# Optimization experiments

Measured on AMD Instinct MI355X. Metric: run time of the kernel, lower is better.

The kernel has to match this reference:

```python
import jax, jax.numpy as jnp
import numpy as np

B, NQ, NK = 2, 1024, 8192
DIM, CTX_DIM = 512, 512
HEADS, DIM_HEAD = 8, 64
INNER = HEADS * DIM_HEAD
EPS = 1e-5
SCALE = DIM_HEAD ** -0.5


def layernorm(x, w, b):
    m = jnp.mean(x, axis=-1, keepdims=True)
    v = jnp.var(x, axis=-1, keepdims=True)
    return (x - m) * jax.lax.rsqrt(v + EPS) * w + b


def rotate_half(x):
    # interleaved pairs: (..., 2i, 2i+1) -> (-x[2i+1], x[2i])
    x1 = x[..., 0::2]
    x2 = x[..., 1::2]
    return jnp.stack((-x2, x1), axis=-1).reshape(x.shape)


def apply_rope(freqs, x):
    # freqs: (b, n, d) broadcast over heads; x: (b, h, n, d)
    f = freqs[:, None, :, :]
    return x * jnp.cos(f) + rotate_half(x) * jnp.sin(f)


def setup_inputs() -> dict:
    key = jax.random.key(0)
    ks = jax.random.split(key, 12)
    x_query = jax.random.normal(ks[0], (B, NQ, DIM), jnp.float32)
    x_context = jax.random.normal(ks[1], (B, NK, CTX_DIM), jnp.float32)
    rotary_q = jax.random.uniform(ks[2], (B, NQ, DIM_HEAD), jnp.float32) * 6.28
    rotary_c = jax.random.uniform(ks[3], (B, NK, DIM_HEAD), jnp.float32) * 6.28
    attn_mask = jax.random.uniform(ks[4], (B, NK)) > 0.1
    attn_mask = attn_mask.at[:, 0].set(True)  # ensure >=1 valid key per row
    s_q = (1.0 / DIM) ** 0.5
    s_c = (1.0 / CTX_DIM) ** 0.5
    s_o = (1.0 / INNER) ** 0.5
    return {
        'x_query': x_query,
        'x_context': x_context,
        'rotary_q': rotary_q,
        'rotary_c': rotary_c,
        'attn_mask': attn_mask,
        'norm_w': jnp.ones((DIM,), jnp.float32),
        'norm_b': jnp.zeros((DIM,), jnp.float32),
        'norm_ctx_w': jnp.ones((CTX_DIM,), jnp.float32),
        'norm_ctx_b': jnp.zeros((CTX_DIM,), jnp.float32),
        'w_q': jax.random.uniform(ks[5], (DIM, INNER), jnp.float32, -s_q, s_q),
        'w_kv': jax.random.uniform(ks[6], (CTX_DIM, 2 * INNER), jnp.float32, -s_c, s_c),
        'w_out': jax.random.uniform(ks[7], (INNER, DIM), jnp.float32, -s_o, s_o),
        'b_out': jax.random.uniform(ks[8], (DIM,), jnp.float32, -s_o, s_o),
    }


def reference(x_query, x_context, rotary_q, rotary_c, attn_mask,
              norm_w, norm_b, norm_ctx_w, norm_ctx_b, w_q, w_kv, w_out, b_out):
    xq = layernorm(x_query, norm_w, norm_b)
    xc = layernorm(x_context, norm_ctx_w, norm_ctx_b)
    q = jnp.einsum('bnd,de->bne', xq, w_q)
    kv = jnp.einsum('bnd,de->bne', xc, w_kv)
    k, v = jnp.split(kv, 2, axis=-1)
    split_heads = lambda t: t.reshape(t.shape[0], t.shape[1], HEADS, DIM_HEAD).transpose(0, 2, 1, 3)
    q, k, v = split_heads(q), split_heads(k), split_heads(v)
    q = apply_rope(rotary_q, q)
    k = apply_rope(rotary_c, k)
    v = apply_rope(rotary_c, v)  # rotate_value=True
    scores = jnp.einsum('bhqd,bhkd->bhqk', q, k) * SCALE
    scores = jnp.where(attn_mask[:, None, None, :], scores, jnp.finfo(scores.dtype).min)
    attn = jax.nn.softmax(scores, axis=-1)
    out = jnp.einsum('bhqk,bhkd->bhqd', attn, v)
    out = apply_rope(-rotary_q, out)  # inverse rotation of output
    out = out.transpose(0, 2, 1, 3).reshape(out.shape[0], NQ, INNER)
    return jnp.einsum('bne,ed->bnd', out, w_out) + b_out
```

## Files before the change

kernel.cpp:

```cpp
#include <hip/hip_runtime.h>
#include <math.h>

typedef __attribute__((ext_vector_type(8))) short  short8;
typedef __attribute__((ext_vector_type(4))) float  f32x4;
typedef __attribute__((ext_vector_type(4))) unsigned short u16x4;
typedef __attribute__((ext_vector_type(8))) unsigned short u16x8;
typedef unsigned short u16;

#define B_     2
#define NQ_    1024
#define NK_    8192
#define DIM_   512
#define H_     8
#define DH_    64
#define EPS_   1e-5f
#define SCALE_ 0.125f
#define LOG2E_ 1.4426950408889634f
#define SPLITS 4

__device__ __forceinline__ u16 f2bf(float f) {
  unsigned int u = __float_as_uint(f);
  u += 0x7fffu + ((u >> 16) & 1u);
  return (u16)(u >> 16);
}
__device__ __forceinline__ float fmax3(float a, float b, float c) {
  return fmaxf(fmaxf(a, b), c);
}

__global__ __launch_bounds__(256) void wt_kernel(
    const float* __restrict__ wq, const float* __restrict__ wkv,
    const float* __restrict__ wout,
    u16* __restrict__ wqT, u16* __restrict__ wkvT, u16* __restrict__ woutT) {
  __shared__ float tile[64][65];
  int bid = blockIdx.x;
  const float* W; u16* WT; int N; int tix;
  if (bid < 64)       { W = wq;   WT = wqT;   N = 512;  tix = bid; }
  else if (bid < 192) { W = wkv;  WT = wkvT;  N = 1024; tix = bid - 64; }
  else                { W = wout; WT = woutT; N = 512;  tix = bid - 192; }
  int ntn = N >> 6;
  int k0 = (tix / ntn) << 6, n0 = (tix % ntn) << 6;
  int t = threadIdx.x;
  {
    int kk = t >> 2, nc = (t & 3) << 4;
#pragma unroll
    for (int i = 0; i < 4; ++i) {
      f32x4 v = *(const f32x4*)&W[(size_t)(k0 + kk) * N + n0 + nc + 4 * i];
      tile[kk][nc + 4*i + 0] = v[0];
      tile[kk][nc + 4*i + 1] = v[1];
      tile[kk][nc + 4*i + 2] = v[2];
      tile[kk][nc + 4*i + 3] = v[3];
    }
  }
  __syncthreads();
  {
    int n = t >> 2, kc = (t & 3) << 4;
#pragma unroll
    for (int i = 0; i < 2; ++i) {
      u16x8 o;
#pragma unroll
      for (int j = 0; j < 8; ++j) o[j] = f2bf(tile[kc + 8*i + j][n]);
      *(u16x8*)&WT[(size_t)(n0 + n) * 512 + k0 + kc + 8*i] = o;
    }
  }
}

__global__ __launch_bounds__(256) void ln_kernel(
    const float* __restrict__ xq, const float* __restrict__ xc,
    const float* __restrict__ nw, const float* __restrict__ nb,
    const float* __restrict__ ncw, const float* __restrict__ ncb,
    u16* __restrict__ xqb, u16* __restrict__ xcb) {
  int wid = threadIdx.x >> 6, lane = threadIdx.x & 63;
  int row = blockIdx.x * 4 + wid;
  const float* x; const float* w; const float* bb; u16* o; int r;
  if (row < 2048) { x = xq; w = nw;  bb = nb;  o = xqb; r = row; }
  else            { x = xc; w = ncw; bb = ncb; o = xcb; r = row - 2048; }
  const f32x4* px = (const f32x4*)(x + (size_t)r * 512);
  f32x4 v0 = px[lane], v1 = px[lane + 64];
  float s  = v0[0]+v0[1]+v0[2]+v0[3] + v1[0]+v1[1]+v1[2]+v1[3];
  float ss = v0[0]*v0[0]+v0[1]*v0[1]+v0[2]*v0[2]+v0[3]*v0[3]
           + v1[0]*v1[0]+v1[1]*v1[1]+v1[2]*v1[2]+v1[3]*v1[3];
#pragma unroll
  for (int ofs = 32; ofs >= 1; ofs >>= 1) { s += __shfl_xor(s, ofs); ss += __shfl_xor(ss, ofs); }
  float mu = s * (1.f/512.f);
  float var = ss * (1.f/512.f) - mu*mu;
  float rs = rsqrtf(var + EPS_);
  const f32x4* pw = (const f32x4*)w; const f32x4* pb = (const f32x4*)bb;
#pragma unroll
  for (int seg = 0; seg < 2; ++seg) {
    int e4 = lane + 64*seg;
    f32x4 xv = seg ? v1 : v0;
    f32x4 wv = pw[e4], bv = pb[e4];
    u16x4 ov;
#pragma unroll
    for (int c = 0; c < 4; ++c) ov[c] = f2bf((xv[c]-mu)*rs*wv[c] + bv[c]);
    *(u16x4*)&o[(size_t)r*512 + e4*4] = ov;
  }
}

__global__ __launch_bounds__(256) void trig_kernel(
    const float* __restrict__ rq, const float* __restrict__ rc,
    float* __restrict__ cq, float* __restrict__ sq,
    float* __restrict__ cc, float* __restrict__ sc) {
  int i = blockIdx.x * 256 + threadIdx.x;
  const int NQE = B_*NQ_*DH_;
  const int NCE = B_*NK_*DH_;
  if (i < NQE) { float s, c; sincosf(rq[i], &s, &c); cq[i] = c; sq[i] = s; }
  if (i < NCE) { float s, c; sincosf(rc[i], &s, &c); cc[i] = c; sc[i] = s; }
}

template<int MODE>
__global__ __launch_bounds__(256) void gemm_mfma(
    const u16* __restrict__ Abf, const u16* __restrict__ WT,
    const float* __restrict__ ctab, const float* __restrict__ stab,
    const float* __restrict__ bias,
    u16* __restrict__ out0, u16* __restrict__ out1, float* __restrict__ outf) {
  constexpr int BM   = (MODE==1) ? 128 : 64;
  constexpr int BN   = (MODE==1) ? 128 : 32;
  constexpr int MR   = BM/64;
  constexpr int NR   = BN/16;
  constexpr int N    = (MODE==1) ? 1024 : 512;
  constexpr int NSEQ = (MODE==1) ? 8192 : 1024;
  constexpr int NBN  = N / BN;
  constexpr int NWG  = (((MODE==1)?16384:2048)/BM) * NBN;
  __shared__ u16 As[BM*64];
  __shared__ u16 Bs[BN*64];
  const int tid = threadIdx.x;
  const int w = tid >> 6, l = tid & 63;
  const int la = l >> 4, lb = l & 15;
  int bid = blockIdx.x;
  bid = (bid & 7) * (NWG/8) + (bid >> 3);
  const int m0 = (bid / NBN) * BM;
  const int n0 = (bid % NBN) * BN;
  f32x4 acc[MR][NR];
#pragma unroll
  for (int i = 0; i < MR; ++i)
#pragma unroll
    for (int j = 0; j < NR; ++j) acc[i][j] = (f32x4){0.f,0.f,0.f,0.f};

  constexpr int APT = BM/32;
  constexpr int BPT = BN/32;
  const int arow = tid / (8/APT);
  const int ag0  = (tid % (8/APT)) * APT;
  const int brow = tid / (8/BPT);
  const int bg0  = (tid % (8/BPT)) * BPT;

  auto loadA = [&](int k0, int g) -> short8 {
    if (MODE == 2) {
      int kk = k0 + g*8;
      int m = m0 + arow;
      return *(const short8*)&Abf[((size_t)((m >> 10)*H_ + (kk >> 6)) * NQ_ + (m & 1023)) * 64 + (kk & 63)];
    } else {
      return *(const short8*)&Abf[(size_t)(m0 + arow) * 512 + k0 + g*8];
    }
  };

  short8 apre[APT], bpre[BPT];
#pragma unroll
  for (int i = 0; i < APT; ++i) apre[i] = loadA(0, ag0 + i);
#pragma unroll
  for (int i = 0; i < BPT; ++i) bpre[i] = *(const short8*)&WT[(size_t)(n0 + brow) * 512 + (bg0 + i)*8];

  for (int k0 = 0; k0 < 512; k0 += 64) {
    if (k0) __syncthreads();
#pragma unroll
    for (int i = 0; i < APT; ++i) {
      int g = ag0 + i;
      *(short8*)&As[arow*64 + ((g ^ (arow & 7)) << 3)] = apre[i];
    }
#pragma unroll
    for (int i = 0; i < BPT; ++i) {
      int g = bg0 + i;
      *(short8*)&Bs[brow*64 + ((g ^ (brow & 7)) << 3)] = bpre[i];
    }
    if (k0 + 64 < 512) {
#pragma unroll
      for (int i = 0; i < APT; ++i) apre[i] = loadA(k0 + 64, ag0 + i);
#pragma unroll
      for (int i = 0; i < BPT; ++i) bpre[i] = *(const short8*)&WT[(size_t)(n0 + brow) * 512 + (k0+64) + (bg0 + i)*8];
    }
    __syncthreads();
#pragma unroll
    for (int h = 0; h < 2; ++h) {
      short8 af[MR], bfr[NR];
#pragma unroll
      for (int i = 0; i < MR; ++i) {
        int row = w*(16*MR) + i*16 + lb;
        int g = (4*h + la) ^ (row & 7);
        af[i] = *(const short8*)&As[row*64 + g*8];
      }
#pragma unroll
      for (int j = 0; j < NR; ++j) {
        int row = j*16 + lb;
        int g = (4*h + la) ^ (row & 7);
        bfr[j] = *(const short8*)&Bs[row*64 + g*8];
      }
#pragma unroll
      for (int i = 0; i < MR; ++i)
#pragma unroll
        for (int j = 0; j < NR; ++j)
          acc[i][j] = __builtin_amdgcn_mfma_f32_16x16x32_bf16(af[i], bfr[j], acc[i][j], 0, 0, 0);
    }
  }

  if (MODE == 2) {
#pragma unroll
    for (int i = 0; i < MR; ++i)
#pragma unroll
      for (int j = 0; j < NR; ++j) {
        int n = n0 + 16*j + lb;
        float bv = bias[n];
#pragma unroll
        for (int r = 0; r < 4; ++r) {
          int m = m0 + w*(16*MR) + 16*i + 4*la + r;
          outf[(size_t)m * 512 + n] = acc[i][j][r] + bv;
        }
      }
  } else if (MODE == 1 && n0 >= 512) {
#pragma unroll
    for (int i = 0; i < MR; ++i)
#pragma unroll
      for (int j = 0; j < NR; ++j) {
        int n = n0 + 16*j + lb;
        int e = n - 512, hh = e >> 6, dh = e & 63;
        int mbase = m0 + w*(16*MR) + 16*i + 4*la;
        int bI = mbase / NSEQ;
        int seq = mbase - bI*NSEQ;
        u16x4 pk4;
#pragma unroll
        for (int r = 0; r < 4; ++r) {
          int m = mbase + r;
          float x = acc[i][j][r];
          float pr = __shfl_xor(x, 1);
          float cv = ctab[(size_t)m*64 + dh];
          float sv = stab[(size_t)m*64 + dh];
          pk4[r] = f2bf(x*cv + ((n & 1) ? pr*sv : -pr*sv));
        }
        *(u16x4*)&out1[((size_t)(bI*H_ + hh)*64 + dh)*8192 + seq] = pk4;
      }
  } else {
#pragma unroll
    for (int i = 0; i < MR; ++i)
#pragma unroll
      for (int j = 0; j < NR; ++j) {
        int n = n0 + 16*j + lb;
        int hh = n >> 6, dh = n & 63;
#pragma unroll
        for (int r = 0; r < 4; ++r) {
          int m = m0 + w*(16*MR) + 16*i + 4*la + r;
          float x = acc[i][j][r];
          float pr = __shfl_xor(x, 1);
          float cv = ctab[(size_t)m*64 + dh];
          float sv = stab[(size_t)m*64 + dh];
          float y = x*cv + ((n & 1) ? pr*sv : -pr*sv);
          if (MODE == 0) y *= SCALE_ * LOG2E_;
          int bI = m / NSEQ, seq = m % NSEQ;
          out0[((size_t)(bI*H_ + hh) * NSEQ + seq) * 64 + dh] = f2bf(y);
        }
      }
  }
}

__global__ __launch_bounds__(512) void attn_mfma(
    const u16* __restrict__ qb, const u16* __restrict__ kb,
    const u16* __restrict__ vtg, const int* __restrict__ mask,
    float* __restrict__ Opart, float* __restrict__ mpart, float* __restrict__ lpart) {
  __shared__ u16 Ks[64*64];
  __shared__ u16 Vt[64*64];
  __shared__ u16 Ps[8*16*64];
  __shared__ float Mskf[2048];
  int bid = blockIdx.x;
  bid = (bid & 7) * 64 + (bid >> 3);
  const int s  = bid & (SPLITS-1);
  const int qt = (bid >> 2) & 7;
  const int bh = bid >> 5;
  const int bI = bh >> 3;
  const int tid = threadIdx.x;
  const int w = tid >> 6, l = tid & 63;
  const int la = l >> 4, lb = l & 15;
  const int key0 = s * (NK_/SPLITS);

#pragma unroll
  for (int i = 0; i < 4; ++i)
    Mskf[i*512 + tid] = mask[bI*NK_ + key0 + i*512 + tid] ? 0.f : -1e30f;

  const int qrow = qt*128 + w*16 + lb;
  short8 qf0 = *(const short8*)&qb[(((size_t)bh * NQ_) + qrow) * 64 + 8*la];
  short8 qf1 = *(const short8*)&qb[(((size_t)bh * NQ_) + qrow) * 64 + 32 + 8*la];

  const int krow = tid >> 3;
  const int kg   = tid & 7;
  const u16* kptr = kb  + ((size_t)bh * NK_ + key0 + krow) * 64;
  const u16* vptr = vtg + ((size_t)bh * 64 + krow) * 8192 + key0;
  short8 kpre = *(const short8*)&kptr[kg*8];
  short8 vpre = *(const short8*)&vptr[kg*8];
  const int ksw = krow & 7;

  f32x4 accO[4];
#pragma unroll
  for (int j = 0; j < 4; ++j) accO[j] = (f32x4){0.f,0.f,0.f,0.f};
  float m_run = -1e30f, l_run = 0.f;
  constexpr int NT = (NK_/SPLITS)/64;

  const int pbase = (w*16 + lb)*64;
  const int pwofs = (4*la) & 7;

  for (int kt = 0; kt < NT; ++kt) {
    *(short8*)&Ks[krow*64 + ((kg ^ ksw) << 3)] = kpre;
    *(short8*)&Vt[krow*64 + ((kg ^ ksw) << 3)] = vpre;
    if (kt + 1 < NT) {
      kpre = *(const short8*)&kptr[(kt+1)*4096 + kg*8];
      vpre = *(const short8*)&vptr[(kt+1)*64 + kg*8];
    }
    __syncthreads();

    f32x4 sc[4];
#pragma unroll
    for (int t = 0; t < 4; ++t) sc[t] = (f32x4){0.f,0.f,0.f,0.f};
    __builtin_amdgcn_s_setprio(1);
#pragma unroll
    for (int t = 0; t < 4; ++t) {
      int row = t*16 + lb;
      int g0 = la ^ (row & 7);
      int g1 = (4 + la) ^ (row & 7);
      short8 kf0 = *(const short8*)&Ks[row*64 + g0*8];
      short8 kf1 = *(const short8*)&Ks[row*64 + g1*8];
      sc[t] = __builtin_amdgcn_mfma_f32_16x16x32_bf16(kf0, qf0, sc[t], 0, 0, 0);
      sc[t] = __builtin_amdgcn_mfma_f32_16x16x32_bf16(kf1, qf1, sc[t], 0, 0, 0);
    }
    __builtin_amdgcn_s_setprio(0);
    float sv[16];
#pragma unroll
    for (int t = 0; t < 4; ++t) {
      f32x4 mk = *(const f32x4*)&Mskf[kt*64 + t*16 + 4*la];
#pragma unroll
      for (int r = 0; r < 4; ++r) sv[4*t+r] = sc[t][r] + mk[r];
    }
    float a0 = fmax3(sv[0],  sv[1],  sv[2]);
    float a1 = fmax3(sv[3],  sv[4],  sv[5]);
    float a2 = fmax3(sv[6],  sv[7],  sv[8]);
    float a3 = fmax3(sv[9],  sv[10], sv[11]);
    float a4 = fmax3(sv[12], sv[13], sv[14]);
    float pmax = fmaxf(fmax3(a0, a1, a2), fmax3(a3, a4, sv[15]));
    pmax = fmaxf(pmax, __shfl_xor(pmax, 16));
    pmax = fmaxf(pmax, __shfl_xor(pmax, 32));
    if (!__all(pmax <= m_run + 11.f)) {
      float mnew = fmaxf(m_run, pmax);
      float scl = __builtin_amdgcn_exp2f(m_run - mnew);
      m_run = mnew;
      l_run *= scl;
      float sr[4];
#pragma unroll
      for (int r = 0; r < 4; ++r) sr[r] = __shfl(scl, (l & 48) | (4*la + r));
#pragma unroll
      for (int j = 0; j < 4; ++j)
#pragma unroll
        for (int r = 0; r < 4; ++r) accO[j][r] *= sr[r];
    }
    float p[16];
    float psum = 0.f;
#pragma unroll
    for (int i = 0; i < 16; ++i) {
      p[i] = __builtin_amdgcn_exp2f(sv[i] - m_run);
      psum += p[i];
    }
    psum += __shfl_xor(psum, 16);
    psum += __shfl_xor(psum, 32);
    l_run += psum;
#pragma unroll
    for (int t = 0; t < 4; ++t) {
      int gst = 2*t + (la >> 1);
      uint2 pp;
      asm("v_cvt_pk_bf16_f32 %0, %1, %2" : "=v"(pp.x) : "v"(p[4*t+0]), "v"(p[4*t+1]));
      asm("v_cvt_pk_bf16_f32 %0, %1, %2" : "=v"(pp.y) : "v"(p[4*t+2]), "v"(p[4*t+3]));
      *(uint2*)&Ps[pbase + ((gst ^ (lb & 7)) << 3) + pwofs] = pp;
    }
    __builtin_amdgcn_s_setprio(1);
#pragma unroll
    for (int kh = 0; kh < 2; ++kh) {
      int pg = (4*kh + la) ^ (lb & 7);
      short8 pf = *(const short8*)&Ps[pbase + pg*8];
#pragma unroll
      for (int j = 0; j < 4; ++j) {
        int d = j*16 + lb;
        int vg = (4*kh + la) ^ (d & 7);
        short8 vf = *(const short8*)&Vt[d*64 + vg*8];
        accO[j] = __builtin_amdgcn_mfma_f32_16x16x32_bf16(pf, vf, accO[j], 0, 0, 0);
      }
    }
    __builtin_amdgcn_s_setprio(0);
    __syncthreads();
  }

  const int qa = qt*128 + w*16;
  const size_t obase = ((size_t)s*16 + bh) * 1024;
#pragma unroll
  for (int j = 0; j < 4; ++j)
#pragma unroll
    for (int r = 0; r < 4; ++r)
      Opart[(obase + qa + 4*la + r) * 64 + j*16 + lb] = accO[j][r];
  if (la == 0) {
    mpart[obase + qa + lb] = m_run;
    lpart[obase + qa + lb] = l_run;
  }
}

__global__ __launch_bounds__(256) void combine_kernel(
    const float* __restrict__ Opart, const float* __restrict__ mpart,
    const float* __restrict__ lpart,
    const float* __restrict__ cosq, const float* __restrict__ sinq,
    u16* __restrict__ aob) {
  const int bid = blockIdx.x;
  const int bh = bid >> 4, qt = bid & 15;
  const int t = threadIdx.x;
  const int ql = t >> 2, ds = (t & 3) << 4;
  const int q = qt*64 + ql;
  const int bI = bh >> 3;
  const size_t rbase = ((size_t)bh << 10) + q;
  float m[SPLITS], li[SPLITS];
  float M = -1e30f;
#pragma unroll
  for (int s = 0; s < SPLITS; ++s) {
    m[s]  = mpart[(size_t)s*16384 + rbase];
    li[s] = lpart[(size_t)s*16384 + rbase];
    M = fmaxf(M, m[s]);
  }
  float ws[SPLITS]; float den = 0.f;
#pragma unroll
  for (int s = 0; s < SPLITS; ++s) { ws[s] = __builtin_amdgcn_exp2f(m[s] - M); den += ws[s]*li[s]; }
  float inv = 1.f / den;
  u16 ob[16];
#pragma unroll
  for (int c = 0; c < 4; ++c) {
    int d0 = ds + 4*c;
    f32x4 o = (f32x4){0.f,0.f,0.f,0.f};
#pragma unroll
    for (int s = 0; s < SPLITS; ++s) {
      f32x4 v = *(const f32x4*)&Opart[((size_t)s*16384 + rbase)*64 + d0];
      o += ws[s] * v;
    }
    o *= inv;
    size_t tix = ((((size_t)bI << 10) + q) << 6) + d0;
    f32x4 cv = *(const f32x4*)&cosq[tix];
    f32x4 sv = *(const f32x4*)&sinq[tix];
    ob[4*c+0] = f2bf(o[0]*cv[0] + o[1]*sv[0]);
    ob[4*c+1] = f2bf(o[1]*cv[1] - o[0]*sv[1]);
    ob[4*c+2] = f2bf(o[2]*cv[2] + o[3]*sv[2]);
    ob[4*c+3] = f2bf(o[3]*cv[3] - o[2]*sv[3]);
  }
  u16x8 w0, w1;
#pragma unroll
  for (int j = 0; j < 8; ++j) { w0[j] = ob[j]; w1[j] = ob[8+j]; }
  *(u16x8*)&aob[rbase*64 + ds]     = w0;
  *(u16x8*)&aob[rbase*64 + ds + 8] = w1;
}

extern "C" void kernel_launch(void* const* d_in, const int* in_sizes, int n_in,
                              void* d_out, int out_size, void* d_ws, size_t ws_size,
                              hipStream_t stream) {
  (void)in_sizes; (void)n_in; (void)out_size; (void)ws_size;
  const float* xq   = (const float*)d_in[0];
  const float* xc   = (const float*)d_in[1];
  const float* rq   = (const float*)d_in[2];
  const float* rc   = (const float*)d_in[3];
  const int*   mask = (const int*)d_in[4];
  const float* nw   = (const float*)d_in[5];
  const float* nb   = (const float*)d_in[6];
  const float* ncw  = (const float*)d_in[7];
  const float* ncb  = (const float*)d_in[8];
  const float* wq   = (const float*)d_in[9];
  const float* wkv  = (const float*)d_in[10];
  const float* wout = (const float*)d_in[11];
  const float* bout = (const float*)d_in[12];
  float* out = (float*)d_out;

  char* p = (char*)d_ws;
  u16* wqT   = (u16*)p;  p += 524288;
  u16* wkvT  = (u16*)p;  p += 1048576;
  u16* woutT = (u16*)p;  p += 524288;
  u16* xqb   = (u16*)p;  p += 2097152;
  u16* xcb   = (u16*)p;  p += 16777216;
  float* cosq = (float*)p; p += 524288;
  float* sinq = (float*)p; p += 524288;
  float* cosc = (float*)p; p += 4194304;
  float* sinc = (float*)p; p += 4194304;
  u16* qb  = (u16*)p; p += 2097152;
  u16* kb  = (u16*)p; p += 16777216;
  u16* vtg = (u16*)p; p += 16777216;
  float* mpart = (float*)p; p += 262144;
  float* lpart = (float*)p; p += 262144;
  u16* aob = (u16*)p; p += 2097152;
  float* Opart = (float*)xcb;

  wt_kernel<<<dim3(256), dim3(256), 0, stream>>>(wq, wkv, wout, wqT, wkvT, woutT);
  ln_kernel<<<dim3(4608), dim3(256), 0, stream>>>(xq, xc, nw, nb, ncw, ncb, xqb, xcb);
  trig_kernel<<<dim3(4096), dim3(256), 0, stream>>>(rq, rc, cosq, sinq, cosc, sinc);
  gemm_mfma<0><<<dim3(512), dim3(256), 0, stream>>>(
      xqb, wqT, cosq, sinq, nullptr, qb, nullptr, nullptr);
  gemm_mfma<1><<<dim3(1024), dim3(256), 0, stream>>>(
      xcb, wkvT, cosc, sinc, nullptr, kb, vtg, nullptr);
  attn_mfma<<<dim3(16*8*SPLITS), dim3(512), 0, stream>>>(
      qb, kb, vtg, mask, Opart, mpart, lpart);
  combine_kernel<<<dim3(256), dim3(256), 0, stream>>>(
      Opart, mpart, lpart, cosq, sinq, aob);
  gemm_mfma<2><<<dim3(512), dim3(256), 0, stream>>>(
      aob, woutT, nullptr, nullptr, bout, nullptr, nullptr, out);
}
```

Measured before the change: 213.0 us.

## Fuse prep kernels, fold key mask into V, and use 8-way KV split

```diff
diff --git a/kernel.cpp b/kernel.cpp
--- a/kernel.cpp
+++ b/kernel.cpp
@@ -16,7 +16,6 @@
 #define EPS_   1e-5f
 #define SCALE_ 0.125f
 #define LOG2E_ 1.4426950408889634f
-#define SPLITS 4
 
 __device__ __forceinline__ u16 f2bf(float f) {
   unsigned int u = __float_as_uint(f);
@@ -27,92 +26,95 @@
   return fmaxf(fmaxf(a, b), c);
 }
 
-__global__ __launch_bounds__(256) void wt_kernel(
+__global__ __launch_bounds__(256) void prep_kernel(
     const float* __restrict__ wq, const float* __restrict__ wkv,
     const float* __restrict__ wout,
-    u16* __restrict__ wqT, u16* __restrict__ wkvT, u16* __restrict__ woutT) {
-  __shared__ float tile[64][65];
-  int bid = blockIdx.x;
-  const float* W; u16* WT; int N; int tix;
-  if (bid < 64)       { W = wq;   WT = wqT;   N = 512;  tix = bid; }
-  else if (bid < 192) { W = wkv;  WT = wkvT;  N = 1024; tix = bid - 64; }
-  else                { W = wout; WT = woutT; N = 512;  tix = bid - 192; }
-  int ntn = N >> 6;
-  int k0 = (tix / ntn) << 6, n0 = (tix % ntn) << 6;
-  int t = threadIdx.x;
-  {
-    int kk = t >> 2, nc = (t & 3) << 4;
-#pragma unroll
-    for (int i = 0; i < 4; ++i) {
-      f32x4 v = *(const f32x4*)&W[(size_t)(k0 + kk) * N + n0 + nc + 4 * i];
-      tile[kk][nc + 4*i + 0] = v[0];
-      tile[kk][nc + 4*i + 1] = v[1];
-      tile[kk][nc + 4*i + 2] = v[2];
-      tile[kk][nc + 4*i + 3] = v[3];
-    }
-  }
-  __syncthreads();
-  {
-    int n = t >> 2, kc = (t & 3) << 4;
-#pragma unroll
-    for (int i = 0; i < 2; ++i) {
-      u16x8 o;
-#pragma unroll
-      for (int j = 0; j < 8; ++j) o[j] = f2bf(tile[kc + 8*i + j][n]);
-      *(u16x8*)&WT[(size_t)(n0 + n) * 512 + k0 + kc + 8*i] = o;
-    }
-  }
-}
-
-__global__ __launch_bounds__(256) void ln_kernel(
     const float* __restrict__ xq, const float* __restrict__ xc,
     const float* __restrict__ nw, const float* __restrict__ nb,
     const float* __restrict__ ncw, const float* __restrict__ ncb,
-    u16* __restrict__ xqb, u16* __restrict__ xcb) {
-  int wid = threadIdx.x >> 6, lane = threadIdx.x & 63;
-  int row = blockIdx.x * 4 + wid;
-  const float* x; const float* w; const float* bb; u16* o; int r;
-  if (row < 2048) { x = xq; w = nw;  bb = nb;  o = xqb; r = row; }
-  else            { x = xc; w = ncw; bb = ncb; o = xcb; r = row - 2048; }
-  const f32x4* px = (const f32x4*)(x + (size_t)r * 512);
-  f32x4 v0 = px[lane], v1 = px[lane + 64];
-  float s  = v0[0]+v0[1]+v0[2]+v0[3] + v1[0]+v1[1]+v1[2]+v1[3];
-  float ss = v0[0]*v0[0]+v0[1]*v0[1]+v0[2]*v0[2]+v0[3]*v0[3]
-           + v1[0]*v1[0]+v1[1]*v1[1]+v1[2]*v1[2]+v1[3]*v1[3];
-#pragma unroll
-  for (int ofs = 32; ofs >= 1; ofs >>= 1) { s += __shfl_xor(s, ofs); ss += __shfl_xor(ss, ofs); }
-  float mu = s * (1.f/512.f);
-  float var = ss * (1.f/512.f) - mu*mu;
-  float rs = rsqrtf(var + EPS_);
-  const f32x4* pw = (const f32x4*)w; const f32x4* pb = (const f32x4*)bb;
-#pragma unroll
-  for (int seg = 0; seg < 2; ++seg) {
-    int e4 = lane + 64*seg;
-    f32x4 xv = seg ? v1 : v0;
-    f32x4 wv = pw[e4], bv = pb[e4];
-    u16x4 ov;
-#pragma unroll
-    for (int c = 0; c < 4; ++c) ov[c] = f2bf((xv[c]-mu)*rs*wv[c] + bv[c]);
-    *(u16x4*)&o[(size_t)r*512 + e4*4] = ov;
-  }
-}
-
-__global__ __launch_bounds__(256) void trig_kernel(
     const float* __restrict__ rq, const float* __restrict__ rc,
-    float* __restrict__ cq, float* __restrict__ sq,
-    float* __restrict__ cc, float* __restrict__ sc) {
-  int i = blockIdx.x * 256 + threadIdx.x;
-  const int NQE = B_*NQ_*DH_;
-  const int NCE = B_*NK_*DH_;
-  if (i < NQE) { float s, c; sincosf(rq[i], &s, &c); cq[i] = c; sq[i] = s; }
-  if (i < NCE) { float s, c; sincosf(rc[i], &s, &c); cc[i] = c; sc[i] = s; }
+    const int* __restrict__ mask,
+    u16* __restrict__ wqT, u16* __restrict__ wkvT, u16* __restrict__ woutT,
+    u16* __restrict__ xqb, u16* __restrict__ xcb,
+    float* __restrict__ cq, float* __restrict__ sq2,
+    float* __restrict__ cc, float* __restrict__ sc2,
+    float* __restrict__ maskf) {
+  __shared__ float tile[64][65];
+  const int bid = blockIdx.x;
+  const int t = threadIdx.x;
+  if (bid < 256) {
+    const float* W; u16* WT; int N; int tix;
+    if (bid < 64)       { W = wq;   WT = wqT;   N = 512;  tix = bid; }
+    else if (bid < 192) { W = wkv;  WT = wkvT;  N = 1024; tix = bid - 64; }
+    else                { W = wout; WT = woutT; N = 512;  tix = bid - 192; }
+    int ntn = N >> 6;
+    int k0 = (tix / ntn) << 6, n0 = (tix % ntn) << 6;
+    {
+      int kk = t >> 2, nc = (t & 3) << 4;
+#pragma unroll
+      for (int i = 0; i < 4; ++i) {
+        f32x4 v = *(const f32x4*)&W[(size_t)(k0 + kk) * N + n0 + nc + 4 * i];
+        tile[kk][nc + 4*i + 0] = v[0];
+        tile[kk][nc + 4*i + 1] = v[1];
+        tile[kk][nc + 4*i + 2] = v[2];
+        tile[kk][nc + 4*i + 3] = v[3];
+      }
+    }
+    __syncthreads();
+    {
+      int n = t >> 2, kc = (t & 3) << 4;
+#pragma unroll
+      for (int i = 0; i < 2; ++i) {
+        u16x8 o;
+#pragma unroll
+        for (int j = 0; j < 8; ++j) o[j] = f2bf(tile[kc + 8*i + j][n]);
+        *(u16x8*)&WT[(size_t)(n0 + n) * 512 + k0 + kc + 8*i] = o;
+      }
+    }
+  } else if (bid < 4864) {
+    int wid = t >> 6, lane = t & 63;
+    int row = (bid - 256) * 4 + wid;
+    const float* x; const float* w; const float* bb; u16* o; int r;
+    if (row < 2048) { x = xq; w = nw;  bb = nb;  o = xqb; r = row; }
+    else            { x = xc; w = ncw; bb = ncb; o = xcb; r = row - 2048; }
+    const f32x4* px = (const f32x4*)(x + (size_t)r * 512);
+    f32x4 v0 = px[lane], v1 = px[lane + 64];
+    float s  = v0[0]+v0[1]+v0[2]+v0[3] + v1[0]+v1[1]+v1[2]+v1[3];
+    float ss = v0[0]*v0[0]+v0[1]*v0[1]+v0[2]*v0[2]+v0[3]*v0[3]
+             + v1[0]*v1[0]+v1[1]*v1[1]+v1[2]*v1[2]+v1[3]*v1[3];
+#pragma unroll
+    for (int ofs = 32; ofs >= 1; ofs >>= 1) { s += __shfl_xor(s, ofs); ss += __shfl_xor(ss, ofs); }
+    float mu = s * (1.f/512.f);
+    float var = ss * (1.f/512.f) - mu*mu;
+    float rs = rsqrtf(var + EPS_);
+    const f32x4* pw = (const f32x4*)w; const f32x4* pb = (const f32x4*)bb;
+#pragma unroll
+    for (int seg = 0; seg < 2; ++seg) {
+      int e4 = lane + 64*seg;
+      f32x4 xv = seg ? v1 : v0;
+      f32x4 wv = pw[e4], bv = pb[e4];
+      u16x4 ov;
+#pragma unroll
+      for (int c = 0; c < 4; ++c) ov[c] = f2bf((xv[c]-mu)*rs*wv[c] + bv[c]);
+      *(u16x4*)&o[(size_t)r*512 + e4*4] = ov;
+    }
+  } else if (bid < 8960) {
+    int i = (bid - 4864) * 256 + t;
+    const int NQE = B_*NQ_*DH_;
+    const int NCE = B_*NK_*DH_;
+    if (i < NQE) { float s, c; sincosf(rq[i], &s, &c); cq[i] = c; sq2[i] = s; }
+    if (i < NCE) { float s, c; sincosf(rc[i], &s, &c); cc[i] = c; sc2[i] = s; }
+  } else {
+    int i = (bid - 8960) * 256 + t;
+    maskf[i] = mask[i] ? 1.f : 0.f;
+  }
 }
 
 template<int MODE>
 __global__ __launch_bounds__(256) void gemm_mfma(
     const u16* __restrict__ Abf, const u16* __restrict__ WT,
     const float* __restrict__ ctab, const float* __restrict__ stab,
-    const float* __restrict__ bias,
+    const float* __restrict__ bias, const float* __restrict__ mvf,
     u16* __restrict__ out0, u16* __restrict__ out1, float* __restrict__ outf) {
   constexpr int BM   = (MODE==1) ? 128 : 64;
   constexpr int BN   = (MODE==1) ? 128 : 32;
@@ -217,14 +219,15 @@
       }
   } else if (MODE == 1 && n0 >= 512) {
 #pragma unroll
-    for (int i = 0; i < MR; ++i)
+    for (int i = 0; i < MR; ++i) {
+      int mbase = m0 + w*(16*MR) + 16*i + 4*la;
+      int bI = mbase >> 13;
+      int seq = mbase & 8191;
+      f32x4 mkv = *(const f32x4*)&mvf[mbase];
 #pragma unroll
       for (int j = 0; j < NR; ++j) {
         int n = n0 + 16*j + lb;
         int e = n - 512, hh = e >> 6, dh = e & 63;
-        int mbase = m0 + w*(16*MR) + 16*i + 4*la;
-        int bI = mbase / NSEQ;
-        int seq = mbase - bI*NSEQ;
         u16x4 pk4;
 #pragma unroll
         for (int r = 0; r < 4; ++r) {
@@ -233,10 +236,11 @@
           float pr = __shfl_xor(x, 1);
           float cv = ctab[(size_t)m*64 + dh];
           float sv = stab[(size_t)m*64 + dh];
-          pk4[r] = f2bf(x*cv + ((n & 1) ? pr*sv : -pr*sv));
+          pk4[r] = f2bf((x*cv + ((n & 1) ? pr*sv : -pr*sv)) * mkv[r]);
         }
         *(u16x4*)&out1[((size_t)(bI*H_ + hh)*64 + dh)*8192 + seq] = pk4;
       }
+    }
   } else {
 #pragma unroll
     for (int i = 0; i < MR; ++i)
@@ -260,28 +264,27 @@
   }
 }
 
+template<int NS>
 __global__ __launch_bounds__(512) void attn_mfma(
     const u16* __restrict__ qb, const u16* __restrict__ kb,
-    const u16* __restrict__ vtg, const int* __restrict__ mask,
+    const u16* __restrict__ vtg, const float* __restrict__ maskf,
     float* __restrict__ Opart, float* __restrict__ mpart, float* __restrict__ lpart) {
   __shared__ u16 Ks[64*64];
   __shared__ u16 Vt[64*64];
   __shared__ u16 Ps[8*16*64];
-  __shared__ float Mskf[2048];
-  int bid = blockIdx.x;
-  bid = (bid & 7) * 64 + (bid >> 3);
-  const int s  = bid & (SPLITS-1);
-  const int qt = (bid >> 2) & 7;
-  const int bh = bid >> 5;
+  constexpr int NWG = 16*8*NS;
+  constexpr int CH  = NWG/8;
+  constexpr int LS  = (NS==8) ? 3 : 2;
+  int orig = blockIdx.x;
+  int wid = (orig & 7) * CH + (orig >> 3);
+  const int qt = wid & 7;
+  const int s  = (wid >> 3) & (NS-1);
+  const int bh = wid >> (3 + LS);
   const int bI = bh >> 3;
   const int tid = threadIdx.x;
   const int w = tid >> 6, l = tid & 63;
   const int la = l >> 4, lb = l & 15;
-  const int key0 = s * (NK_/SPLITS);
-
-#pragma unroll
-  for (int i = 0; i < 4; ++i)
-    Mskf[i*512 + tid] = mask[bI*NK_ + key0 + i*512 + tid] ? 0.f : -1e30f;
+  const int key0 = s * (NK_/NS);
 
   const int qrow = qt*128 + w*16 + lb;
   short8 qf0 = *(const short8*)&qb[(((size_t)bh * NQ_) + qrow) * 64 + 8*la];
@@ -294,12 +297,13 @@
   short8 kpre = *(const short8*)&kptr[kg*8];
   short8 vpre = *(const short8*)&vptr[kg*8];
   const int ksw = krow & 7;
+  const float* mrow = maskf + bI*8192 + key0 + 4*la;
 
   f32x4 accO[4];
 #pragma unroll
   for (int j = 0; j < 4; ++j) accO[j] = (f32x4){0.f,0.f,0.f,0.f};
   float m_run = -1e30f, l_run = 0.f;
-  constexpr int NT = (NK_/SPLITS)/64;
+  constexpr int NT = (NK_/NS)/64;
 
   const int pbase = (w*16 + lb)*64;
   const int pwofs = (4*la) & 7;
@@ -328,19 +332,12 @@
       sc[t] = __builtin_amdgcn_mfma_f32_16x16x32_bf16(kf1, qf1, sc[t], 0, 0, 0);
     }
     __builtin_amdgcn_s_setprio(0);
-    float sv[16];
-#pragma unroll
-    for (int t = 0; t < 4; ++t) {
-      f32x4 mk = *(const f32x4*)&Mskf[kt*64 + t*16 + 4*la];
-#pragma unroll
-      for (int r = 0; r < 4; ++r) sv[4*t+r] = sc[t][r] + mk[r];
-    }
-    float a0 = fmax3(sv[0],  sv[1],  sv[2]);
-    float a1 = fmax3(sv[3],  sv[4],  sv[5]);
-    float a2 = fmax3(sv[6],  sv[7],  sv[8]);
-    float a3 = fmax3(sv[9],  sv[10], sv[11]);
-    float a4 = fmax3(sv[12], sv[13], sv[14]);
-    float pmax = fmaxf(fmax3(a0, a1, a2), fmax3(a3, a4, sv[15]));
+    float a0 = fmax3(sc[0][0], sc[0][1], sc[0][2]);
+    float a1 = fmax3(sc[0][3], sc[1][0], sc[1][1]);
+    float a2 = fmax3(sc[1][2], sc[1][3], sc[2][0]);
+    float a3 = fmax3(sc[2][1], sc[2][2], sc[2][3]);
+    float a4 = fmax3(sc[3][0], sc[3][1], sc[3][2]);
+    float pmax = fmaxf(fmax3(a0, a1, a2), fmax3(a3, a4, sc[3][3]));
     pmax = fmaxf(pmax, __shfl_xor(pmax, 16));
     pmax = fmaxf(pmax, __shfl_xor(pmax, 32));
     if (!__all(pmax <= m_run + 11.f)) {
@@ -356,24 +353,25 @@
 #pragma unroll
         for (int r = 0; r < 4; ++r) accO[j][r] *= sr[r];
     }
-    float p[16];
-    float psum = 0.f;
-#pragma unroll
-    for (int i = 0; i < 16; ++i) {
-      p[i] = __builtin_amdgcn_exp2f(sv[i] - m_run);
-      psum += p[i];
-    }
-    psum += __shfl_xor(psum, 16);
-    psum += __shfl_xor(psum, 32);
-    l_run += psum;
+    float l_add = 0.f;
 #pragma unroll
     for (int t = 0; t < 4; ++t) {
+      f32x4 mk = *(const f32x4*)&mrow[kt*64 + t*16];
+      float p0 = __builtin_amdgcn_exp2f(sc[t][0] - m_run);
+      float p1 = __builtin_amdgcn_exp2f(sc[t][1] - m_run);
+      float p2 = __builtin_amdgcn_exp2f(sc[t][2] - m_run);
+      float p3 = __builtin_amdgcn_exp2f(sc[t][3] - m_run);
+      l_add = fmaf(p0, mk[0], l_add);
+      l_add = fmaf(p1, mk[1], l_add);
+      l_add = fmaf(p2, mk[2], l_add);
+      l_add = fmaf(p3, mk[3], l_add);
       int gst = 2*t + (la >> 1);
       uint2 pp;
-      asm("v_cvt_pk_bf16_f32 %0, %1, %2" : "=v"(pp.x) : "v"(p[4*t+0]), "v"(p[4*t+1]));
-      asm("v_cvt_pk_bf16_f32 %0, %1, %2" : "=v"(pp.y) : "v"(p[4*t+2]), "v"(p[4*t+3]));
+      asm("v_cvt_pk_bf16_f32 %0, %1, %2" : "=v"(pp.x) : "v"(p0), "v"(p1));
+      asm("v_cvt_pk_bf16_f32 %0, %1, %2" : "=v"(pp.y) : "v"(p2), "v"(p3));
       *(uint2*)&Ps[pbase + ((gst ^ (lb & 7)) << 3) + pwofs] = pp;
     }
+    l_run += l_add;
     __builtin_amdgcn_s_setprio(1);
 #pragma unroll
     for (int kh = 0; kh < 2; ++kh) {
@@ -391,6 +389,9 @@
     __syncthreads();
   }
 
+  l_run += __shfl_xor(l_run, 16);
+  l_run += __shfl_xor(l_run, 32);
+
   const int qa = qt*128 + w*16;
   const size_t obase = ((size_t)s*16 + bh) * 1024;
 #pragma unroll
@@ -404,6 +405,7 @@
   }
 }
 
+template<int NS>
 __global__ __launch_bounds__(256) void combine_kernel(
     const float* __restrict__ Opart, const float* __restrict__ mpart,
     const float* __restrict__ lpart,
@@ -416,17 +418,17 @@
   const int q = qt*64 + ql;
   const int bI = bh >> 3;
   const size_t rbase = ((size_t)bh << 10) + q;
-  float m[SPLITS], li[SPLITS];
+  float m[NS], li[NS];
   float M = -1e30f;
 #pragma unroll
-  for (int s = 0; s < SPLITS; ++s) {
+  for (int s = 0; s < NS; ++s) {
     m[s]  = mpart[(size_t)s*16384 + rbase];
     li[s] = lpart[(size_t)s*16384 + rbase];
     M = fmaxf(M, m[s]);
   }
-  float ws[SPLITS]; float den = 0.f;
-#pragma unroll
-  for (int s = 0; s < SPLITS; ++s) { ws[s] = __builtin_amdgcn_exp2f(m[s] - M); den += ws[s]*li[s]; }
+  float ws[NS]; float den = 0.f;
+#pragma unroll
+  for (int s = 0; s < NS; ++s) { ws[s] = __builtin_amdgcn_exp2f(m[s] - M); den += ws[s]*li[s]; }
   float inv = 1.f / den;
   u16 ob[16];
 #pragma unroll
@@ -434,7 +436,7 @@
     int d0 = ds + 4*c;
     f32x4 o = (f32x4){0.f,0.f,0.f,0.f};
 #pragma unroll
-    for (int s = 0; s < SPLITS; ++s) {
+    for (int s = 0; s < NS; ++s) {
       f32x4 v = *(const f32x4*)&Opart[((size_t)s*16384 + rbase)*64 + d0];
       o += ws[s] * v;
     }
@@ -457,7 +459,7 @@
 extern "C" void kernel_launch(void* const* d_in, const int* in_sizes, int n_in,
                               void* d_out, int out_size, void* d_ws, size_t ws_size,
                               hipStream_t stream) {
-  (void)in_sizes; (void)n_in; (void)out_size; (void)ws_size;
+  (void)in_sizes; (void)n_in; (void)out_size;
   const float* xq   = (const float*)d_in[0];
   const float* xc   = (const float*)d_in[1];
   const float* rq   = (const float*)d_in[2];
@@ -474,34 +476,47 @@
   float* out = (float*)d_out;
 
   char* p = (char*)d_ws;
-  u16* wqT   = (u16*)p;  p += 524288;
-  u16* wkvT  = (u16*)p;  p += 1048576;
-  u16* woutT = (u16*)p;  p += 524288;
-  u16* xqb   = (u16*)p;  p += 2097152;
-  u16* xcb   = (u16*)p;  p += 16777216;
-  float* cosq = (float*)p; p += 524288;
-  float* sinq = (float*)p; p += 524288;
-  float* cosc = (float*)p; p += 4194304;
-  float* sinc = (float*)p; p += 4194304;
-  u16* qb  = (u16*)p; p += 2097152;
-  u16* kb  = (u16*)p; p += 16777216;
-  u16* vtg = (u16*)p; p += 16777216;
-  float* mpart = (float*)p; p += 262144;
-  float* lpart = (float*)p; p += 262144;
-  u16* aob = (u16*)p; p += 2097152;
-  float* Opart = (float*)xcb;
-
-  wt_kernel<<<dim3(256), dim3(256), 0, stream>>>(wq, wkv, wout, wqT, wkvT, woutT);
-  ln_kernel<<<dim3(4608), dim3(256), 0, stream>>>(xq, xc, nw, nb, ncw, ncb, xqb, xcb);
-  trig_kernel<<<dim3(4096), dim3(256), 0, stream>>>(rq, rc, cosq, sinq, cosc, sinc);
+  u16*   woutT  = (u16*)p;   p += 524288;
+  float* cosq   = (float*)p; p += 524288;
+  float* sinq   = (float*)p; p += 524288;
+  u16*   qb     = (u16*)p;   p += 2097152;
+  u16*   kb     = (u16*)p;   p += 16777216;
+  u16*   vtg    = (u16*)p;   p += 16777216;
+  float* mpart4 = (float*)p; p += 262144;
+  float* lpart4 = (float*)p; p += 262144;
+  u16*   aob    = (u16*)p;   p += 2097152;
+  float* maskf  = (float*)aob;
+  char* pool = p;
+  u16*   wqT   = (u16*)p;   p += 524288;
+  u16*   wkvT  = (u16*)p;   p += 1048576;
+  u16*   xqb   = (u16*)p;   p += 2097152;
+  u16*   xcb   = (u16*)p;   p += 16777216;
+  float* cosc  = (float*)p; p += 4194304;
+  float* sinc  = (float*)p; p += 4194304;
+  float* Opart = (float*)pool;
+  float* mpart8 = (float*)(pool + 33554432);
+  float* lpart8 = (float*)(pool + 33554432 + 524288);
+  const size_t need8 = (size_t)(pool - (char*)d_ws) + 33554432ull + 1048576ull;
+  const bool use8 = ws_size >= need8;
+
+  prep_kernel<<<dim3(9024), dim3(256), 0, stream>>>(
+      wq, wkv, wout, xq, xc, nw, nb, ncw, ncb, rq, rc, mask,
+      wqT, wkvT, woutT, xqb, xcb, cosq, sinq, cosc, sinc, maskf);
   gemm_mfma<0><<<dim3(512), dim3(256), 0, stream>>>(
-      xqb, wqT, cosq, sinq, nullptr, qb, nullptr, nullptr);
+      xqb, wqT, cosq, sinq, nullptr, nullptr, qb, nullptr, nullptr);
   gemm_mfma<1><<<dim3(1024), dim3(256), 0, stream>>>(
-      xcb, wkvT, cosc, sinc, nullptr, kb, vtg, nullptr);
-  attn_mfma<<<dim3(16*8*SPLITS), dim3(512), 0, stream>>>(
-      qb, kb, vtg, mask, Opart, mpart, lpart);
-  combine_kernel<<<dim3(256), dim3(256), 0, stream>>>(
-      Opart, mpart, lpart, cosq, sinq, aob);
+      xcb, wkvT, cosc, sinc, nullptr, maskf, kb, vtg, nullptr);
+  if (use8) {
+    attn_mfma<8><<<dim3(1024), dim3(512), 0, stream>>>(
+        qb, kb, vtg, maskf, Opart, mpart8, lpart8);
+    combine_kernel<8><<<dim3(256), dim3(256), 0, stream>>>(
+        Opart, mpart8, lpart8, cosq, sinq, aob);
+  } else {
+    attn_mfma<4><<<dim3(512), dim3(512), 0, stream>>>(
+        qb, kb, vtg, maskf, Opart, mpart4, lpart4);
+    combine_kernel<4><<<dim3(256), dim3(256), 0, stream>>>(
+        Opart, mpart4, lpart4, cosq, sinq, aob);
+  }
   gemm_mfma<2><<<dim3(512), dim3(256), 0, stream>>>(
-      aob, woutT, nullptr, nullptr, bout, nullptr, nullptr, out);
-}
+      aob, woutT, nullptr, nullptr, bout, nullptr, nullptr, nullptr, out);
+}
```

New measurement: 209.2 us. Within noise of the previous version (-1.8%).
